# Optimization experiments

Measured on AMD Instinct MI355X. Metric: run time of the kernel, lower is better.

Reference implementation:

```python
import jax, jax.numpy as jnp
import numpy as np

B = 32          # number of trees (batch)
N_LEAVES = 512  # complete binary tree -> 2*N_LEAVES-1 nodes per tree
IN_DIM = 1024
MEM = 1024


def setup_inputs() -> dict:
    key = jax.random.key(0)
    k1, k2, k3, k4 = jax.random.split(key, 4)
    s = 0.02
    inputs = jax.random.normal(k1, (B, N_LEAVES, IN_DIM), jnp.float32)
    w_fioux = jax.random.normal(k2, (4 * MEM, IN_DIM), jnp.float32) * s
    # rand_init: bias zero except first mem_dim entries set to 1 (forget-gate bias)
    b_fioux = jnp.zeros((4 * MEM,), jnp.float32).at[:MEM].set(1.0)
    w_iouh = jax.random.normal(k3, (3 * MEM, 2 * MEM), jnp.float32) * s
    w_fh = jax.random.normal(k4, (2 * MEM, 2 * MEM), jnp.float32) * s
    return {"inputs": inputs, "w_fioux": w_fioux, "b_fioux": b_fioux,
            "w_iouh": w_iouh, "w_fh": w_fh}


def _node_forward(x, child_c, child_h, w_fioux, b_fioux, w_iouh, w_fh):
    # x: [B, n, IN_DIM]; child_c/child_h: [B, n, 2*MEM] (left || right)
    fioux = x @ w_fioux.T + b_fioux                      # [B, n, 4M]
    fx, ix, ox, ux = jnp.split(fioux, 4, axis=-1)        # each [B, n, M]
    ih, oh, uh = jnp.split(child_h @ w_iouh.T, 3, axis=-1)
    i = jax.nn.sigmoid(ix + ih)
    o = jax.nn.sigmoid(ox + oh)
    u = jnp.tanh(ux + uh)
    # f gates: fx repeated for both children + fh(child_h)
    f = jax.nn.sigmoid(jnp.concatenate([fx, fx], axis=-1) + child_h @ w_fh.T)
    fc = f * child_c                                     # [B, n, 2M]
    c = i * u + fc[..., :MEM] + fc[..., MEM:]            # sum over the 2 children
    h = o * jnp.tanh(c)
    return c, h


def reference(inputs, w_fioux, b_fioux, w_iouh, w_fh):
    # Leaves: x = word input, child states are zeros
    z = jnp.zeros((B, N_LEAVES, 2 * MEM), inputs.dtype)
    c, h = _node_forward(inputs, z, z, w_fioux, b_fioux, w_iouh, w_fh)
    n = N_LEAVES
    # Internal nodes, level by level (log2(N_LEAVES) fixed iterations):
    # x = zeros (internal nodes have no token input), children are adjacent pairs.
    while n > 1:
        n //= 2
        child_c = c.reshape(B, n, 2 * MEM)   # [left_c || right_c]
        child_h = h.reshape(B, n, 2 * MEM)
        x = jnp.zeros((B, n, IN_DIM), inputs.dtype)
        c, h = _node_forward(x, child_c, child_h, w_fioux, b_fioux, w_iouh, w_fh)
    return h[:, 0, :]  # root hidden state, [B, MEM]
```

## Files before the change

kernel.cpp:

```cpp
#include <hip/hip_runtime.h>
#include <cstdint>
#include <cstddef>


typedef __attribute__((ext_vector_type(8))) short bf16x8;
typedef __attribute__((ext_vector_type(4))) float f32x4;

__device__ __forceinline__ float sig_(float x) { return 1.0f / (1.0f + __expf(-x)); }

__device__ __forceinline__ unsigned short f2bf_(float x) {
    union { float f; uint32_t u; } v; v.f = x;
    uint32_t r = v.u + 0x7fffu + ((v.u >> 16) & 1u);
    return (unsigned short)(r >> 16);
}
__device__ __forceinline__ float bf2f_(unsigned short u) {
    union { uint32_t u; float f; } v; v.u = ((uint32_t)u) << 16; return v.f;
}

#define GL16(g, l) __builtin_amdgcn_global_load_lds( \
    (const __attribute__((address_space(1))) void*)(g), \
    (__attribute__((address_space(3))) void*)(l), 16, 0, 0)

__global__ __launch_bounds__(512, 2)
void gemm384f(const unsigned short* __restrict__ A,
              const unsigned short* __restrict__ Wp,
              const float* __restrict__ b,
              unsigned short* __restrict__ c_out,
              unsigned short* __restrict__ h_out,
              int M)
{
    __shared__ unsigned short lA[4 * 4096];
    __shared__ unsigned short lB[4 * 12288];
    const int lda = 1024;

    const int orig = blockIdx.x + 8 * blockIdx.y;
    const int bx = orig & 7;
    const int by = orig >> 3;

    const int tid = threadIdx.x;
    const int ln  = tid & 63;
    const int wv  = tid >> 6;
    const int wrp = wv >> 2;
    const int wcp = wv & 3;
    const int row0 = by * 128;
    const int colb = bx * 384;

    const int rowS = tid >> 2;
    const int gS   = (tid & 3) ^ ((tid >> 3) & 3);
    const unsigned short* a0 = A + (size_t)min(row0 + rowS, M - 1) * lda + gS * 8;
    const unsigned short* w0 = Wp + (size_t)(colb + rowS)       * lda + gS * 8;
    const unsigned short* w1 = Wp + (size_t)(colb + rowS + 128) * lda + gS * 8;
    const unsigned short* w2 = Wp + (size_t)(colb + rowS + 256) * lda + gS * 8;
    const int ld0 = tid * 8;
    const int ld1 = tid * 8 + 4096;
    const int ld2 = tid * 8 + 8192;

    int offA[4], offB[6];
    #pragma unroll
    for (int i = 0; i < 4; ++i) {
        const int r = wrp * 64 + i * 16 + (ln & 15);
        offA[i] = r * 32 + ((ln >> 4) ^ ((r >> 1) & 3)) * 8;
    }
    #pragma unroll
    for (int h = 0; h < 2; ++h)
        #pragma unroll
        for (int g = 0; g < 3; ++g) {
            const int r = h * 192 + g * 64 + wcp * 16 + (ln & 15);
            offB[h * 3 + g] = r * 32 + ((ln >> 4) ^ ((r >> 1) & 3)) * 8;
        }

    f32x4 acc[4][6] = {};
    const int P = 32;

#define ISSUE_L(kh) do { \
    const int _sl = (kh) & 3; \
    const size_t _ko = (size_t)(kh) * 32; \
    GL16(a0 + _ko, lA + _sl * 4096 + ld0); \
    GL16(w0 + _ko, lB + _sl * 12288 + ld0); \
    GL16(w1 + _ko, lB + _sl * 12288 + ld1); \
    GL16(w2 + _ko, lB + _sl * 12288 + ld2); \
} while (0)

    ISSUE_L(0); ISSUE_L(1); ISSUE_L(2);
    asm volatile("s_waitcnt vmcnt(8)" ::: "memory");
    asm volatile("s_barrier" ::: "memory");

    for (int p = 0; p < P; ++p) {
        const unsigned short* pa = lA + (p & 3) * 4096;
        const unsigned short* pb = lB + (p & 3) * 12288;
        bf16x8 bf[6], af[4];
        #pragma unroll
        for (int i = 0; i < 6; ++i) bf[i] = *(const bf16x8*)(pb + offB[i]);
        #pragma unroll
        for (int i = 0; i < 4; ++i) af[i] = *(const bf16x8*)(pa + offA[i]);
        if (p <= P - 4) ISSUE_L(p + 3);
        __builtin_amdgcn_s_setprio(1);
        #pragma unroll
        for (int m = 0; m < 4; ++m)
            #pragma unroll
            for (int g = 0; g < 6; ++g)
                acc[m][g] = __builtin_amdgcn_mfma_f32_16x16x32_bf16(af[m], bf[g], acc[m][g], 0, 0, 0);
        __builtin_amdgcn_s_setprio(0);
        if (p <= P - 4)      asm volatile("s_waitcnt vmcnt(8)" ::: "memory");
        else if (p == P - 3) asm volatile("s_waitcnt vmcnt(4)" ::: "memory");
        else if (p == P - 2) asm volatile("s_waitcnt vmcnt(0)" ::: "memory");
        if (p < P - 1) asm volatile("s_barrier" ::: "memory");
    }
#undef ISSUE_L

    #pragma unroll
    for (int h = 0; h < 2; ++h) {
        const int j = bx * 128 + h * 64 + wcp * 16 + (ln & 15);
        const float bi = b[1024 + j];
        const float bo = b[2048 + j];
        const float bu = b[3072 + j];
        #pragma unroll
        for (int mi = 0; mi < 4; ++mi) {
            #pragma unroll
            for (int rg = 0; rg < 4; ++rg) {
                const int r = row0 + wrp * 64 + mi * 16 + (ln >> 4) * 4 + rg;
                if (r < M) {
                    const float cv = sig_(acc[mi][h * 3 + 0][rg] + bi) * tanhf(acc[mi][h * 3 + 2][rg] + bu);
                    const float hv = sig_(acc[mi][h * 3 + 1][rg] + bo) * tanhf(cv);
                    c_out[(size_t)r * 1024 + j] = f2bf_(cv);
                    h_out[(size_t)r * 1024 + j] = f2bf_(hv);
                }
            }
        }
    }
}

__global__ __launch_bounds__(512, 2)
void gemm320f(const unsigned short* __restrict__ A,
              const unsigned short* __restrict__ Wp,
              const float* __restrict__ b,
              const unsigned short* __restrict__ c_prev,
              unsigned short* __restrict__ c_out,
              unsigned short* __restrict__ h_out,
              int M)
{
    __shared__ unsigned short lA[4 * 8192];
    __shared__ unsigned short lB[4 * 10240];
    const int lda = 2048;

    const int orig = blockIdx.x + 16 * blockIdx.y;
    const int xcd  = orig & 7;
    const int pos  = orig >> 3;
    const int bx   = xcd * 2 + (pos & 1);
    const int by   = pos >> 1;

    const int tid = threadIdx.x;
    const int ln  = tid & 63;
    const int wv  = tid >> 6;
    const int wrp = wv >> 2;
    const int wcp = wv & 3;
    const int row0 = by * 256;
    const int colb = bx * 320;
    const bool five = (wv < 4);

    const int rowS = tid >> 2;
    const int gS   = (tid & 3) ^ ((tid >> 3) & 3);
    const unsigned short* a0 = A + (size_t)min(row0 + rowS,       M - 1) * lda + gS * 8;
    const unsigned short* a1 = A + (size_t)min(row0 + rowS + 128, M - 1) * lda + gS * 8;
    const unsigned short* w0 = Wp + (size_t)(colb + rowS)       * lda + gS * 8;
    const unsigned short* w1 = Wp + (size_t)(colb + rowS + 128) * lda + gS * 8;
    const unsigned short* w2 = Wp + (size_t)(colb + 256 + ((tid & 255) >> 2)) * lda + gS * 8;
    const int ld0 = tid * 8;
    const int ld1 = tid * 8 + 4096;
    const int ld2 = (tid & 255) * 8 + 8192;

    int offA[8], offB[5];
    #pragma unroll
    for (int i = 0; i < 8; ++i) {
        const int r = wrp * 128 + i * 16 + (ln & 15);
        offA[i] = r * 32 + ((ln >> 4) ^ ((r >> 1) & 3)) * 8;
    }
    #pragma unroll
    for (int g = 0; g < 5; ++g) {
        const int r = g * 64 + wcp * 16 + (ln & 15);
        offB[g] = r * 32 + ((ln >> 4) ^ ((r >> 1) & 3)) * 8;
    }

    f32x4 acc[8][5] = {};
    const int P = 64;

#define ISSUE_F(kh) do { \
    const int _sl = (kh) & 3; \
    const size_t _ko = (size_t)(kh) * 32; \
    GL16(a0 + _ko, lA + _sl * 8192 + ld0); \
    GL16(a1 + _ko, lA + _sl * 8192 + ld1); \
    GL16(w0 + _ko, lB + _sl * 10240 + ld0); \
    GL16(w1 + _ko, lB + _sl * 10240 + ld1); \
    if (five) GL16(w2 + _ko, lB + _sl * 10240 + ld2); \
} while (0)

    ISSUE_F(0); ISSUE_F(1); ISSUE_F(2);
    if (five) asm volatile("s_waitcnt vmcnt(10)" ::: "memory");
    else      asm volatile("s_waitcnt vmcnt(8)"  ::: "memory");
    asm volatile("s_barrier" ::: "memory");

    for (int p = 0; p < P; ++p) {
        const unsigned short* pa = lA + (p & 3) * 8192;
        const unsigned short* pb = lB + (p & 3) * 10240;
        bf16x8 bf[5], af[4], ag[4];
        #pragma unroll
        for (int g = 0; g < 5; ++g) bf[g] = *(const bf16x8*)(pb + offB[g]);
        #pragma unroll
        for (int i = 0; i < 4; ++i) af[i] = *(const bf16x8*)(pa + offA[i]);
        #pragma unroll
        for (int i = 0; i < 4; ++i) ag[i] = *(const bf16x8*)(pa + offA[4 + i]);
        if (p <= P - 4) ISSUE_F(p + 3);
        __builtin_amdgcn_s_setprio(1);
        #pragma unroll
        for (int m = 0; m < 4; ++m)
            #pragma unroll
            for (int g = 0; g < 5; ++g)
                acc[m][g] = __builtin_amdgcn_mfma_f32_16x16x32_bf16(af[m], bf[g], acc[m][g], 0, 0, 0);
        #pragma unroll
        for (int m = 0; m < 4; ++m)
            #pragma unroll
            for (int g = 0; g < 5; ++g)
                acc[4 + m][g] = __builtin_amdgcn_mfma_f32_16x16x32_bf16(ag[m], bf[g], acc[4 + m][g], 0, 0, 0);
        __builtin_amdgcn_s_setprio(0);
        if (p <= P - 4) {
            if (five) asm volatile("s_waitcnt vmcnt(10)" ::: "memory");
            else      asm volatile("s_waitcnt vmcnt(8)"  ::: "memory");
        } else if (p == P - 3) {
            if (five) asm volatile("s_waitcnt vmcnt(5)" ::: "memory");
            else      asm volatile("s_waitcnt vmcnt(4)" ::: "memory");
        } else if (p == P - 2) {
            asm volatile("s_waitcnt vmcnt(0)" ::: "memory");
        }
        if (p < P - 1) asm volatile("s_barrier" ::: "memory");
    }
#undef ISSUE_F

    const int jg = bx * 64 + wcp * 16 + (ln & 15);
    const float bi = b[1024 + jg];
    const float bo = b[2048 + jg];
    const float bu = b[3072 + jg];
    const float bff = b[jg];
    #pragma unroll
    for (int mi = 0; mi < 8; ++mi) {
        #pragma unroll
        for (int rg = 0; rg < 4; ++rg) {
            const int r = row0 + wrp * 128 + mi * 16 + (ln >> 4) * 4 + rg;
            if (r < M) {
                const float cl = bf2f_(c_prev[(size_t)r * 2048 + jg]);
                const float cr = bf2f_(c_prev[(size_t)r * 2048 + 1024 + jg]);
                const float iv = sig_(acc[mi][0][rg] + bi);
                const float ov = sig_(acc[mi][1][rg] + bo);
                const float uv = tanhf(acc[mi][2][rg] + bu);
                const float flv = sig_(acc[mi][3][rg] + bff);
                const float frv = sig_(acc[mi][4][rg] + bff);
                const float c = iv * uv + flv * cl + frv * cr;
                const float h = ov * tanhf(c);
                c_out[(size_t)r * 1024 + jg] = f2bf_(c);
                h_out[(size_t)r * 1024 + jg] = f2bf_(h);
            }
        }
    }
}

__global__ __launch_bounds__(512, 2)
void gemm256(const unsigned short* __restrict__ A,
             const unsigned short* __restrict__ W,
             unsigned short* __restrict__ C, int M, int N, int lda, int Klen)
{
    __shared__ unsigned short lA[4 * 8192];
    __shared__ unsigned short lB[4 * 8192];

    const int gx = gridDim.x, gy = gridDim.y;
    int id = blockIdx.x + gx * (blockIdx.y + gy * blockIdx.z);
    {
        const int nwg = gx * gy * gridDim.z;
        const int q = nwg >> 3, r = nwg & 7, x = id & 7, i = id >> 3;
        id = (x < r ? x * (q + 1) : r * (q + 1) + (x - r) * q) + i;
    }
    const int bz  = id / (gx * gy);
    const int rem = id - bz * gx * gy;
    const int by  = rem / gx;
    const int bx  = rem - by * gx;

    const int tid = threadIdx.x;
    const int ln  = tid & 63;
    const int wv  = tid >> 6;
    const int wrp = wv >> 2;
    const int wcp = wv & 3;
    const int row0 = by * 256;
    const int colb = bx * 256;
    const int kbase = bz * Klen;
    C += (size_t)bz * M * N;

    const int rowS = tid >> 2;
    const int gS   = (tid & 3) ^ ((tid >> 3) & 3);
    const unsigned short* a0 = A + (size_t)min(row0 + rowS,       M - 1) * lda + kbase + gS * 8;
    const unsigned short* a1 = A + (size_t)min(row0 + rowS + 128, M - 1) * lda + kbase + gS * 8;
    const unsigned short* b0 = W + (size_t)(colb + rowS)       * lda + kbase + gS * 8;
    const unsigned short* b1 = W + (size_t)(colb + rowS + 128) * lda + kbase + gS * 8;
    const int ld0 = tid * 8;
    const int ld1 = tid * 8 + 4096;

    int offA[8], offB[4];
    #pragma unroll
    for (int i = 0; i < 8; ++i) {
        const int r = wrp * 128 + i * 16 + (ln & 15);
        offA[i] = r * 32 + ((ln >> 4) ^ ((r >> 1) & 3)) * 8;
    }
    #pragma unroll
    for (int i = 0; i < 4; ++i) {
        const int r = wcp * 64 + i * 16 + (ln & 15);
        offB[i] = r * 32 + ((ln >> 4) ^ ((r >> 1) & 3)) * 8;
    }

    f32x4 acc[8][4] = {};
    const int P = Klen >> 5;

#define ISSUE_KH(kh) do { \
    const int _sl = (kh) & 3; \
    const size_t _ko = (size_t)(kh) * 32; \
    GL16(a0 + _ko, lA + _sl * 8192 + ld0); \
    GL16(a1 + _ko, lA + _sl * 8192 + ld1); \
    GL16(b0 + _ko, lB + _sl * 8192 + ld0); \
    GL16(b1 + _ko, lB + _sl * 8192 + ld1); \
} while (0)

    ISSUE_KH(0); ISSUE_KH(1); ISSUE_KH(2);
    asm volatile("s_waitcnt vmcnt(8)" ::: "memory");
    asm volatile("s_barrier" ::: "memory");

    for (int p = 0; p < P; ++p) {
        const unsigned short* pa = lA + (p & 3) * 8192;
        const unsigned short* pb = lB + (p & 3) * 8192;
        bf16x8 bf[4], af[4], ag[4];
        #pragma unroll
        for (int i = 0; i < 4; ++i) bf[i] = *(const bf16x8*)(pb + offB[i]);
        #pragma unroll
        for (int i = 0; i < 4; ++i) af[i] = *(const bf16x8*)(pa + offA[i]);
        #pragma unroll
        for (int i = 0; i < 4; ++i) ag[i] = *(const bf16x8*)(pa + offA[4 + i]);
        if (p <= P - 4) ISSUE_KH(p + 3);
        __builtin_amdgcn_s_setprio(1);
        #pragma unroll
        for (int m = 0; m < 4; ++m)
            #pragma unroll
            for (int n = 0; n < 4; ++n)
                acc[m][n] = __builtin_amdgcn_mfma_f32_16x16x32_bf16(af[m], bf[n], acc[m][n], 0, 0, 0);
        #pragma unroll
        for (int m = 0; m < 4; ++m)
            #pragma unroll
            for (int n = 0; n < 4; ++n)
                acc[4 + m][n] = __builtin_amdgcn_mfma_f32_16x16x32_bf16(ag[m], bf[n], acc[4 + m][n], 0, 0, 0);
        __builtin_amdgcn_s_setprio(0);
        if (p <= P - 4)      asm volatile("s_waitcnt vmcnt(8)" ::: "memory");
        else if (p == P - 3) asm volatile("s_waitcnt vmcnt(4)" ::: "memory");
        else if (p == P - 2) asm volatile("s_waitcnt vmcnt(0)" ::: "memory");
        if (p < P - 1) asm volatile("s_barrier" ::: "memory");
    }
#undef ISSUE_KH

    #pragma unroll
    for (int mi = 0; mi < 8; ++mi) {
        #pragma unroll
        for (int ni = 0; ni < 4; ++ni) {
            const int col = colb + wcp * 64 + ni * 16 + (ln & 15);
            #pragma unroll
            for (int rg = 0; rg < 4; ++rg) {
                const int r = row0 + wrp * 128 + mi * 16 + (ln >> 4) * 4 + rg;
                if (r < M) C[(size_t)r * N + col] = f2bf_(acc[mi][ni][rg]);
            }
        }
    }
}

__global__ void f2bf_vec(const float* __restrict__ src, unsigned short* __restrict__ dst, int n4)
{
    const int i = blockIdx.x * blockDim.x + threadIdx.x;
    if (i >= n4) return;
    const float4 v = ((const float4*)src)[i];
    ushort4 o;
    o.x = f2bf_(v.x); o.y = f2bf_(v.y); o.z = f2bf_(v.z); o.w = f2bf_(v.w);
    ((ushort4*)dst)[i] = o;
}

__global__ void build_wfxp(const float* __restrict__ w_fioux,
                           unsigned short* __restrict__ dst, int total4)
{
    const int idx = blockIdx.x * blockDim.x + threadIdx.x;
    if (idx >= total4) return;
    const int rp = idx >> 8;
    const int c4 = (idx & 255) << 2;
    const int t  = rp / 192;
    const int q  = rp - t * 192;
    const int g  = q >> 6;
    const int jj = q & 63;
    const float* src = w_fioux + (size_t)((g + 1) * 1024 + t * 64 + jj) * 1024;
    const float4 v = *(const float4*)(src + c4);
    ushort4 o;
    o.x = f2bf_(v.x); o.y = f2bf_(v.y); o.z = f2bf_(v.z); o.w = f2bf_(v.w);
    *(ushort4*)(dst + (size_t)rp * 1024 + c4) = o;
}

__global__ void build_wcatp(const float* __restrict__ w_iouh, const float* __restrict__ w_fh,
                            unsigned short* __restrict__ dst, int total4)
{
    const int idx = blockIdx.x * blockDim.x + threadIdx.x;
    if (idx >= total4) return;
    const int rp = idx >> 9;
    const int c4 = (idx & 511) << 2;
    const int t  = rp / 320;
    const int q  = rp - t * 320;
    const int g  = q >> 6;
    const int jj = q & 63;
    const int srow = t * 64 + jj;
    const float* src = (g < 3) ? (w_iouh + (size_t)(g * 1024 + srow) * 2048)
                               : (w_fh   + (size_t)((g - 3) * 1024 + srow) * 2048);
    const float4 v = *(const float4*)(src + c4);
    ushort4 o;
    o.x = f2bf_(v.x); o.y = f2bf_(v.y); o.z = f2bf_(v.z); o.w = f2bf_(v.w);
    *(ushort4*)(dst + (size_t)rp * 2048 + c4) = o;
}

__device__ __forceinline__ void acc4_(float* v, ushort4 u) {
    v[0] += bf2f_(u.x); v[1] += bf2f_(u.y); v[2] += bf2f_(u.z); v[3] += bf2f_(u.w);
}

__global__ void node_gates(const unsigned short* __restrict__ g, int S, size_t sstride,
                           const float* __restrict__ b,
                           const unsigned short* __restrict__ c_prev,
                           unsigned short* __restrict__ c_out,
                           unsigned short* __restrict__ h_bf,
                           float* __restrict__ h_f32, int rows)
{
    const int idx = blockIdx.x * blockDim.x + threadIdx.x;
    if (idx >= rows * 256) return;
    const int r = idx >> 8, q = (idx & 255) << 2;
    const int t = q >> 6, jj = q & 63;
    float vi[4] = {}, vo[4] = {}, vu[4] = {}, vfl[4] = {}, vfr[4] = {};
    const unsigned short* gr = g + (size_t)r * 5120 + t * 320 + jj;
    for (int s = 0; s < S; ++s, gr += sstride) {
        acc4_(vi,  *(const ushort4*)(gr));
        acc4_(vo,  *(const ushort4*)(gr + 64));
        acc4_(vu,  *(const ushort4*)(gr + 128));
        acc4_(vfl, *(const ushort4*)(gr + 192));
        acc4_(vfr, *(const ushort4*)(gr + 256));
    }
    const float* bi = b + 1024 + q;
    const float* bo = b + 2048 + q;
    const float* bu = b + 3072 + q;
    const float* bff = b + q;
    const ushort4 clu = *(const ushort4*)(c_prev + (size_t)r * 2048 + q);
    const ushort4 cru = *(const ushort4*)(c_prev + (size_t)r * 2048 + 1024 + q);
    const float cl[4] = { bf2f_(clu.x), bf2f_(clu.y), bf2f_(clu.z), bf2f_(clu.w) };
    const float cr[4] = { bf2f_(cru.x), bf2f_(cru.y), bf2f_(cru.z), bf2f_(cru.w) };

    ushort4 co, ho;
    float cv[4], hv[4];
    #pragma unroll
    for (int e = 0; e < 4; ++e) {
        const float c = sig_(vi[e] + bi[e]) * tanhf(vu[e] + bu[e])
                      + sig_(vfl[e] + bff[e]) * cl[e]
                      + sig_(vfr[e] + bff[e]) * cr[e];
        cv[e] = c;
        hv[e] = sig_(vo[e] + bo[e]) * tanhf(c);
    }
    co.x = f2bf_(cv[0]); co.y = f2bf_(cv[1]); co.z = f2bf_(cv[2]); co.w = f2bf_(cv[3]);
    ho.x = f2bf_(hv[0]); ho.y = f2bf_(hv[1]); ho.z = f2bf_(hv[2]); ho.w = f2bf_(hv[3]);
    *(ushort4*)(c_out + (size_t)r * 1024 + q) = co;
    *(ushort4*)(h_bf + (size_t)r * 1024 + q) = ho;
    if (h_f32) {
        float4 hf; hf.x = hv[0]; hf.y = hv[1]; hf.z = hv[2]; hf.w = hv[3];
        *(float4*)(h_f32 + (size_t)r * 1024 + q) = hf;
    }
}

extern "C" void kernel_launch(void* const* d_in, const int* in_sizes, int n_in,
                              void* d_out, int out_size, void* d_ws, size_t ws_size,
                              hipStream_t stream)
{
    const float* inputs  = (const float*)d_in[0];
    const float* w_fioux = (const float*)d_in[1];
    const float* b_fioux = (const float*)d_in[2];
    const float* w_iouh  = (const float*)d_in[3];
    const float* w_fh    = (const float*)d_in[4];
    float* out = (float*)d_out;

    unsigned short* us    = (unsigned short*)d_ws;
    unsigned short* c_a   = us;
    unsigned short* c_b   = c_a + (size_t)16777216;
    unsigned short* h_a   = c_b + (size_t)8388608;
    unsigned short* h_b   = h_a + (size_t)16777216;
    unsigned short* wfxP  = h_b + (size_t)8388608;
    unsigned short* wcatP = wfxP + (size_t)3145728;
    unsigned short* gbuf  = wcatP + (size_t)10485760;
    unsigned short* x_bf  = gbuf;

    f2bf_vec<<<16384, 256, 0, stream>>>(inputs, x_bf, 4194304);
    build_wfxp<<<3072, 256, 0, stream>>>(w_fioux, wfxP, 786432);
    build_wcatp<<<10240, 256, 0, stream>>>(w_iouh, w_fh, wcatP, 5120 * 512);

    gemm384f<<<dim3(8, 128), 512, 0, stream>>>(x_bf, wfxP, b_fioux, c_a, h_a, 16384);

    unsigned short *hp = h_a, *cp = c_a, *hn = h_b, *cn = c_b;
    for (int n = 256; n >= 64; n >>= 1) {
        const int m = 32 * n;
        gemm320f<<<dim3(16, m / 256), 512, 0, stream>>>(hp, wcatP, b_fioux, cp, cn, hn, m);
        unsigned short* t;
        t = hp; hp = hn; hn = t;
        t = cp; cp = cn; cn = t;
    }

    for (int n = 32; n >= 1; n >>= 1) {
        const int m = 32 * n;
        const int S = (m >= 512) ? 4 : 8;
        const int Klen = 2048 / S;
        gemm256<<<dim3(20, (m + 255) / 256, S), 512, 0, stream>>>(
            hp, wcatP, gbuf, m, 5120, 2048, Klen);
        node_gates<<<m, 256, 0, stream>>>(
            gbuf, S, (size_t)m * 5120, b_fioux, cp, cn, hn,
            (n == 1) ? out : nullptr, m);
        unsigned short* t;
        t = hp; hp = hn; hn = t;
        t = cp; cp = cn; cn = t;
    }
    (void)in_sizes; (void)n_in; (void)out_size; (void)ws_size;
}
```

Before: 693.6 us.

## Shrink fused GEMM tiles to 256-thread blocks with 3-stage pipeline and finer gate interleave

Replaces the leaf and internal-node fused GEMM+gate kernels with smaller-tile versions: 256 threads, 128-row tiles, 192 or 160 columns, and a 3-slot LDS ring with prefetch distance 2 instead of 4 slots and distance 3. The packed weight layouts are re-interleaved in 16-column gate groups to match, and node_gates is updated for the new layout. It also adds XCD-aware block remapping and an s_sleep stagger for half the blocks. The aim is more blocks in flight and smaller LDS per block for better occupancy and load balance, at the cost of less data reuse per tile and a shallower prefetch.

```diff
diff --git a/kernel.cpp b/kernel.cpp
--- a/kernel.cpp
+++ b/kernel.cpp
@@ -21,242 +21,234 @@
     (const __attribute__((address_space(1))) void*)(g), \
     (__attribute__((address_space(3))) void*)(l), 16, 0, 0)
 
-__global__ __launch_bounds__(512, 2)
-void gemm384f(const unsigned short* __restrict__ A,
-              const unsigned short* __restrict__ Wp,
-              const float* __restrict__ b,
-              unsigned short* __restrict__ c_out,
-              unsigned short* __restrict__ h_out,
-              int M)
-{
-    __shared__ unsigned short lA[4 * 4096];
-    __shared__ unsigned short lB[4 * 12288];
-    const int lda = 1024;
-
-    const int orig = blockIdx.x + 8 * blockIdx.y;
-    const int bx = orig & 7;
-    const int by = orig >> 3;
+__global__ __launch_bounds__(256, 2)
+void gemm_nodef(const unsigned short* __restrict__ A,
+                const unsigned short* __restrict__ Wp,
+                const float* __restrict__ b,
+                const unsigned short* __restrict__ c_prev,
+                unsigned short* __restrict__ c_out,
+                unsigned short* __restrict__ h_out,
+                int M)
+{
+    __shared__ unsigned short lA[3 * 4096];
+    __shared__ unsigned short lB[3 * 5120];
+    const int lda = 2048;
+
+    const int orig = blockIdx.x + 32 * blockIdx.y;
+    const int xcd  = orig & 7;
+    const int pos  = orig >> 3;
+    const int bx   = xcd * 4 + (pos & 3);
+    const int by   = pos >> 2;
+
+    if ((pos >> 5) & 1) asm volatile("s_sleep 10" ::: "memory");
 
     const int tid = threadIdx.x;
     const int ln  = tid & 63;
     const int wv  = tid >> 6;
-    const int wrp = wv >> 2;
-    const int wcp = wv & 3;
+    const int wrp = wv >> 1;
+    const int wcp = wv & 1;
     const int row0 = by * 128;
-    const int colb = bx * 384;
+    const int colb = bx * 160;
+    const bool five = (wv < 2);
 
     const int rowS = tid >> 2;
     const int gS   = (tid & 3) ^ ((tid >> 3) & 3);
-    const unsigned short* a0 = A + (size_t)min(row0 + rowS, M - 1) * lda + gS * 8;
-    const unsigned short* w0 = Wp + (size_t)(colb + rowS)       * lda + gS * 8;
-    const unsigned short* w1 = Wp + (size_t)(colb + rowS + 128) * lda + gS * 8;
-    const unsigned short* w2 = Wp + (size_t)(colb + rowS + 256) * lda + gS * 8;
+    const unsigned short* a0 = A + (size_t)(row0 + rowS) * lda + gS * 8;
+    const unsigned short* a1 = a0 + (size_t)64 * lda;
+    const unsigned short* w0 = Wp + (size_t)(colb + rowS) * lda + gS * 8;
+    const unsigned short* w1 = w0 + (size_t)64 * lda;
+    const unsigned short* w2 = w0 + (size_t)128 * lda;
     const int ld0 = tid * 8;
-    const int ld1 = tid * 8 + 4096;
-    const int ld2 = tid * 8 + 8192;
-
-    int offA[4], offB[6];
+
+    int offA[4], offB[5];
     #pragma unroll
     for (int i = 0; i < 4; ++i) {
         const int r = wrp * 64 + i * 16 + (ln & 15);
         offA[i] = r * 32 + ((ln >> 4) ^ ((r >> 1) & 3)) * 8;
     }
     #pragma unroll
-    for (int h = 0; h < 2; ++h)
-        #pragma unroll
-        for (int g = 0; g < 3; ++g) {
-            const int r = h * 192 + g * 64 + wcp * 16 + (ln & 15);
-            offB[h * 3 + g] = r * 32 + ((ln >> 4) ^ ((r >> 1) & 3)) * 8;
-        }
-
-    f32x4 acc[4][6] = {};
-    const int P = 32;
-
-#define ISSUE_L(kh) do { \
-    const int _sl = (kh) & 3; \
+    for (int g = 0; g < 5; ++g) {
+        const int r = wcp * 80 + g * 16 + (ln & 15);
+        offB[g] = r * 32 + ((ln >> 4) ^ ((r >> 1) & 3)) * 8;
+    }
+
+    f32x4 acc[4][5] = {};
+    const int P = 64;
+
+#define ISSUE_N(sl, kh) do { \
     const size_t _ko = (size_t)(kh) * 32; \
-    GL16(a0 + _ko, lA + _sl * 4096 + ld0); \
-    GL16(w0 + _ko, lB + _sl * 12288 + ld0); \
-    GL16(w1 + _ko, lB + _sl * 12288 + ld1); \
-    GL16(w2 + _ko, lB + _sl * 12288 + ld2); \
+    GL16(a0 + _ko, lA + (sl) * 4096 + ld0); \
+    GL16(a1 + _ko, lA + (sl) * 4096 + 2048 + ld0); \
+    GL16(w0 + _ko, lB + (sl) * 5120 + ld0); \
+    GL16(w1 + _ko, lB + (sl) * 5120 + 2048 + ld0); \
+    if (five) GL16(w2 + _ko, lB + (sl) * 5120 + 4096 + ld0); \
 } while (0)
 
-    ISSUE_L(0); ISSUE_L(1); ISSUE_L(2);
-    asm volatile("s_waitcnt vmcnt(8)" ::: "memory");
+    ISSUE_N(0, 0); ISSUE_N(1, 1);
+    if (five) asm volatile("s_waitcnt vmcnt(5)" ::: "memory");
+    else      asm volatile("s_waitcnt vmcnt(4)" ::: "memory");
     asm volatile("s_barrier" ::: "memory");
 
+    int rd = 0, is = 2;
     for (int p = 0; p < P; ++p) {
-        const unsigned short* pa = lA + (p & 3) * 4096;
-        const unsigned short* pb = lB + (p & 3) * 12288;
-        bf16x8 bf[6], af[4];
-        #pragma unroll
-        for (int i = 0; i < 6; ++i) bf[i] = *(const bf16x8*)(pb + offB[i]);
+        const unsigned short* pa = lA + rd * 4096;
+        const unsigned short* pb = lB + rd * 5120;
+        bf16x8 bf[5], af[4];
+        #pragma unroll
+        for (int g = 0; g < 5; ++g) bf[g] = *(const bf16x8*)(pb + offB[g]);
         #pragma unroll
         for (int i = 0; i < 4; ++i) af[i] = *(const bf16x8*)(pa + offA[i]);
-        if (p <= P - 4) ISSUE_L(p + 3);
-        __builtin_amdgcn_s_setprio(1);
-        #pragma unroll
-        for (int m = 0; m < 4; ++m)
-            #pragma unroll
-            for (int g = 0; g < 6; ++g)
-                acc[m][g] = __builtin_amdgcn_mfma_f32_16x16x32_bf16(af[m], bf[g], acc[m][g], 0, 0, 0);
-        __builtin_amdgcn_s_setprio(0);
-        if (p <= P - 4)      asm volatile("s_waitcnt vmcnt(8)" ::: "memory");
-        else if (p == P - 3) asm volatile("s_waitcnt vmcnt(4)" ::: "memory");
-        else if (p == P - 2) asm volatile("s_waitcnt vmcnt(0)" ::: "memory");
-        if (p < P - 1) asm volatile("s_barrier" ::: "memory");
-    }
-#undef ISSUE_L
-
-    #pragma unroll
-    for (int h = 0; h < 2; ++h) {
-        const int j = bx * 128 + h * 64 + wcp * 16 + (ln & 15);
-        const float bi = b[1024 + j];
-        const float bo = b[2048 + j];
-        const float bu = b[3072 + j];
-        #pragma unroll
-        for (int mi = 0; mi < 4; ++mi) {
-            #pragma unroll
-            for (int rg = 0; rg < 4; ++rg) {
-                const int r = row0 + wrp * 64 + mi * 16 + (ln >> 4) * 4 + rg;
-                if (r < M) {
-                    const float cv = sig_(acc[mi][h * 3 + 0][rg] + bi) * tanhf(acc[mi][h * 3 + 2][rg] + bu);
-                    const float hv = sig_(acc[mi][h * 3 + 1][rg] + bo) * tanhf(cv);
-                    c_out[(size_t)r * 1024 + j] = f2bf_(cv);
-                    h_out[(size_t)r * 1024 + j] = f2bf_(hv);
-                }
-            }
-        }
-    }
-}
-
-__global__ __launch_bounds__(512, 2)
-void gemm320f(const unsigned short* __restrict__ A,
-              const unsigned short* __restrict__ Wp,
-              const float* __restrict__ b,
-              const unsigned short* __restrict__ c_prev,
-              unsigned short* __restrict__ c_out,
-              unsigned short* __restrict__ h_out,
-              int M)
-{
-    __shared__ unsigned short lA[4 * 8192];
-    __shared__ unsigned short lB[4 * 10240];
-    const int lda = 2048;
-
-    const int orig = blockIdx.x + 16 * blockIdx.y;
-    const int xcd  = orig & 7;
-    const int pos  = orig >> 3;
-    const int bx   = xcd * 2 + (pos & 1);
-    const int by   = pos >> 1;
-
-    const int tid = threadIdx.x;
-    const int ln  = tid & 63;
-    const int wv  = tid >> 6;
-    const int wrp = wv >> 2;
-    const int wcp = wv & 3;
-    const int row0 = by * 256;
-    const int colb = bx * 320;
-    const bool five = (wv < 4);
-
-    const int rowS = tid >> 2;
-    const int gS   = (tid & 3) ^ ((tid >> 3) & 3);
-    const unsigned short* a0 = A + (size_t)min(row0 + rowS,       M - 1) * lda + gS * 8;
-    const unsigned short* a1 = A + (size_t)min(row0 + rowS + 128, M - 1) * lda + gS * 8;
-    const unsigned short* w0 = Wp + (size_t)(colb + rowS)       * lda + gS * 8;
-    const unsigned short* w1 = Wp + (size_t)(colb + rowS + 128) * lda + gS * 8;
-    const unsigned short* w2 = Wp + (size_t)(colb + 256 + ((tid & 255) >> 2)) * lda + gS * 8;
-    const int ld0 = tid * 8;
-    const int ld1 = tid * 8 + 4096;
-    const int ld2 = (tid & 255) * 8 + 8192;
-
-    int offA[8], offB[5];
-    #pragma unroll
-    for (int i = 0; i < 8; ++i) {
-        const int r = wrp * 128 + i * 16 + (ln & 15);
-        offA[i] = r * 32 + ((ln >> 4) ^ ((r >> 1) & 3)) * 8;
-    }
-    #pragma unroll
-    for (int g = 0; g < 5; ++g) {
-        const int r = g * 64 + wcp * 16 + (ln & 15);
-        offB[g] = r * 32 + ((ln >> 4) ^ ((r >> 1) & 3)) * 8;
-    }
-
-    f32x4 acc[8][5] = {};
-    const int P = 64;
-
-#define ISSUE_F(kh) do { \
-    const int _sl = (kh) & 3; \
-    const size_t _ko = (size_t)(kh) * 32; \
-    GL16(a0 + _ko, lA + _sl * 8192 + ld0); \
-    GL16(a1 + _ko, lA + _sl * 8192 + ld1); \
-    GL16(w0 + _ko, lB + _sl * 10240 + ld0); \
-    GL16(w1 + _ko, lB + _sl * 10240 + ld1); \
-    if (five) GL16(w2 + _ko, lB + _sl * 10240 + ld2); \
-} while (0)
-
-    ISSUE_F(0); ISSUE_F(1); ISSUE_F(2);
-    if (five) asm volatile("s_waitcnt vmcnt(10)" ::: "memory");
-    else      asm volatile("s_waitcnt vmcnt(8)"  ::: "memory");
-    asm volatile("s_barrier" ::: "memory");
-
-    for (int p = 0; p < P; ++p) {
-        const unsigned short* pa = lA + (p & 3) * 8192;
-        const unsigned short* pb = lB + (p & 3) * 10240;
-        bf16x8 bf[5], af[4], ag[4];
-        #pragma unroll
-        for (int g = 0; g < 5; ++g) bf[g] = *(const bf16x8*)(pb + offB[g]);
-        #pragma unroll
-        for (int i = 0; i < 4; ++i) af[i] = *(const bf16x8*)(pa + offA[i]);
-        #pragma unroll
-        for (int i = 0; i < 4; ++i) ag[i] = *(const bf16x8*)(pa + offA[4 + i]);
-        if (p <= P - 4) ISSUE_F(p + 3);
+        if (p <= P - 3) ISSUE_N(is, p + 2);
         __builtin_amdgcn_s_setprio(1);
         #pragma unroll
         for (int m = 0; m < 4; ++m)
             #pragma unroll
             for (int g = 0; g < 5; ++g)
                 acc[m][g] = __builtin_amdgcn_mfma_f32_16x16x32_bf16(af[m], bf[g], acc[m][g], 0, 0, 0);
-        #pragma unroll
-        for (int m = 0; m < 4; ++m)
-            #pragma unroll
-            for (int g = 0; g < 5; ++g)
-                acc[4 + m][g] = __builtin_amdgcn_mfma_f32_16x16x32_bf16(ag[m], bf[g], acc[4 + m][g], 0, 0, 0);
         __builtin_amdgcn_s_setprio(0);
-        if (p <= P - 4) {
-            if (five) asm volatile("s_waitcnt vmcnt(10)" ::: "memory");
-            else      asm volatile("s_waitcnt vmcnt(8)"  ::: "memory");
-        } else if (p == P - 3) {
+        if (p <= P - 3) {
             if (five) asm volatile("s_waitcnt vmcnt(5)" ::: "memory");
             else      asm volatile("s_waitcnt vmcnt(4)" ::: "memory");
         } else if (p == P - 2) {
             asm volatile("s_waitcnt vmcnt(0)" ::: "memory");
         }
         if (p < P - 1) asm volatile("s_barrier" ::: "memory");
-    }
-#undef ISSUE_F
-
-    const int jg = bx * 64 + wcp * 16 + (ln & 15);
+        rd = (rd == 2) ? 0 : rd + 1;
+        is = (is == 2) ? 0 : is + 1;
+    }
+#undef ISSUE_N
+
+    const int jg = bx * 32 + wcp * 16 + (ln & 15);
     const float bi = b[1024 + jg];
     const float bo = b[2048 + jg];
     const float bu = b[3072 + jg];
     const float bff = b[jg];
     #pragma unroll
-    for (int mi = 0; mi < 8; ++mi) {
+    for (int mi = 0; mi < 4; ++mi) {
         #pragma unroll
         for (int rg = 0; rg < 4; ++rg) {
-            const int r = row0 + wrp * 128 + mi * 16 + (ln >> 4) * 4 + rg;
-            if (r < M) {
-                const float cl = bf2f_(c_prev[(size_t)r * 2048 + jg]);
-                const float cr = bf2f_(c_prev[(size_t)r * 2048 + 1024 + jg]);
-                const float iv = sig_(acc[mi][0][rg] + bi);
-                const float ov = sig_(acc[mi][1][rg] + bo);
-                const float uv = tanhf(acc[mi][2][rg] + bu);
-                const float flv = sig_(acc[mi][3][rg] + bff);
-                const float frv = sig_(acc[mi][4][rg] + bff);
-                const float c = iv * uv + flv * cl + frv * cr;
-                const float h = ov * tanhf(c);
-                c_out[(size_t)r * 1024 + jg] = f2bf_(c);
-                h_out[(size_t)r * 1024 + jg] = f2bf_(h);
+            const int r = row0 + wrp * 64 + mi * 16 + (ln >> 4) * 4 + rg;
+            const float cl = bf2f_(c_prev[(size_t)r * 2048 + jg]);
+            const float cr = bf2f_(c_prev[(size_t)r * 2048 + 1024 + jg]);
+            const float iv = sig_(acc[mi][0][rg] + bi);
+            const float ov = sig_(acc[mi][1][rg] + bo);
+            const float uv = tanhf(acc[mi][2][rg] + bu);
+            const float flv = sig_(acc[mi][3][rg] + bff);
+            const float frv = sig_(acc[mi][4][rg] + bff);
+            const float c = iv * uv + flv * cl + frv * cr;
+            const float h = ov * tanhf(c);
+            c_out[(size_t)r * 1024 + jg] = f2bf_(c);
+            h_out[(size_t)r * 1024 + jg] = f2bf_(h);
+        }
+    }
+}
+
+__global__ __launch_bounds__(256, 2)
+void gemm_leaff(const unsigned short* __restrict__ A,
+                const unsigned short* __restrict__ Wp,
+                const float* __restrict__ b,
+                unsigned short* __restrict__ c_out,
+                unsigned short* __restrict__ h_out)
+{
+    __shared__ unsigned short lA[3 * 4096];
+    __shared__ unsigned short lB[3 * 6144];
+    const int lda = 1024;
+
+    const int orig = blockIdx.x + 16 * blockIdx.y;
+    const int xcd  = orig & 7;
+    const int pos  = orig >> 3;
+    const int bx   = xcd * 2 + (pos & 1);
+    const int by   = pos >> 1;
+
+    if ((pos >> 5) & 1) asm volatile("s_sleep 10" ::: "memory");
+
+    const int tid = threadIdx.x;
+    const int ln  = tid & 63;
+    const int wv  = tid >> 6;
+    const int wrp = wv >> 1;
+    const int wcp = wv & 1;
+    const int row0 = by * 128;
+    const int colb = bx * 192;
+
+    const int rowS = tid >> 2;
+    const int gS   = (tid & 3) ^ ((tid >> 3) & 3);
+    const unsigned short* a0 = A + (size_t)(row0 + rowS) * lda + gS * 8;
+    const unsigned short* a1 = a0 + (size_t)64 * lda;
+    const unsigned short* w0 = Wp + (size_t)(colb + rowS) * lda + gS * 8;
+    const unsigned short* w1 = w0 + (size_t)64 * lda;
+    const unsigned short* w2 = w0 + (size_t)128 * lda;
+    const int ld0 = tid * 8;
+
+    int offA[4], offB[6];
+    #pragma unroll
+    for (int i = 0; i < 4; ++i) {
+        const int r = wrp * 64 + i * 16 + (ln & 15);
+        offA[i] = r * 32 + ((ln >> 4) ^ ((r >> 1) & 3)) * 8;
+    }
+    #pragma unroll
+    for (int grp = 0; grp < 2; ++grp)
+        #pragma unroll
+        for (int g = 0; g < 3; ++g) {
+            const int r = wcp * 96 + grp * 48 + g * 16 + (ln & 15);
+            offB[grp * 3 + g] = r * 32 + ((ln >> 4) ^ ((r >> 1) & 3)) * 8;
+        }
+
+    f32x4 acc[4][6] = {};
+    const int P = 32;
+
+#define ISSUE_L(sl, kh) do { \
+    const size_t _ko = (size_t)(kh) * 32; \
+    GL16(a0 + _ko, lA + (sl) * 4096 + ld0); \
+    GL16(a1 + _ko, lA + (sl) * 4096 + 2048 + ld0); \
+    GL16(w0 + _ko, lB + (sl) * 6144 + ld0); \
+    GL16(w1 + _ko, lB + (sl) * 6144 + 2048 + ld0); \
+    GL16(w2 + _ko, lB + (sl) * 6144 + 4096 + ld0); \
+} while (0)
+
+    ISSUE_L(0, 0); ISSUE_L(1, 1);
+    asm volatile("s_waitcnt vmcnt(5)" ::: "memory");
+    asm volatile("s_barrier" ::: "memory");
+
+    int rd = 0, is = 2;
+    for (int p = 0; p < P; ++p) {
+        const unsigned short* pa = lA + rd * 4096;
+        const unsigned short* pb = lB + rd * 6144;
+        bf16x8 bf[6], af[4];
+        #pragma unroll
+        for (int g = 0; g < 6; ++g) bf[g] = *(const bf16x8*)(pb + offB[g]);
+        #pragma unroll
+        for (int i = 0; i < 4; ++i) af[i] = *(const bf16x8*)(pa + offA[i]);
+        if (p <= P - 3) ISSUE_L(is, p + 2);
+        __builtin_amdgcn_s_setprio(1);
+        #pragma unroll
+        for (int m = 0; m < 4; ++m)
+            #pragma unroll
+            for (int g = 0; g < 6; ++g)
+                acc[m][g] = __builtin_amdgcn_mfma_f32_16x16x32_bf16(af[m], bf[g], acc[m][g], 0, 0, 0);
+        __builtin_amdgcn_s_setprio(0);
+        if (p <= P - 3)      asm volatile("s_waitcnt vmcnt(5)" ::: "memory");
+        else if (p == P - 2) asm volatile("s_waitcnt vmcnt(0)" ::: "memory");
+        if (p < P - 1) asm volatile("s_barrier" ::: "memory");
+        rd = (rd == 2) ? 0 : rd + 1;
+        is = (is == 2) ? 0 : is + 1;
+    }
+#undef ISSUE_L
+
+    #pragma unroll
+    for (int grp = 0; grp < 2; ++grp) {
+        const int j = bx * 64 + wcp * 32 + grp * 16 + (ln & 15);
+        const float bi = b[1024 + j];
+        const float bo = b[2048 + j];
+        const float bu = b[3072 + j];
+        #pragma unroll
+        for (int mi = 0; mi < 4; ++mi) {
+            #pragma unroll
+            for (int rg = 0; rg < 4; ++rg) {
+                const int r = row0 + wrp * 64 + mi * 16 + (ln >> 4) * 4 + rg;
+                const float cv = sig_(acc[mi][grp * 3 + 0][rg] + bi) * tanhf(acc[mi][grp * 3 + 2][rg] + bu);
+                const float hv = sig_(acc[mi][grp * 3 + 1][rg] + bo) * tanhf(cv);
+                c_out[(size_t)r * 1024 + j] = f2bf_(cv);
+                h_out[(size_t)r * 1024 + j] = f2bf_(hv);
             }
         }
     }
@@ -390,11 +382,11 @@
     if (idx >= total4) return;
     const int rp = idx >> 8;
     const int c4 = (idx & 255) << 2;
-    const int t  = rp / 192;
-    const int q  = rp - t * 192;
-    const int g  = q >> 6;
-    const int jj = q & 63;
-    const float* src = w_fioux + (size_t)((g + 1) * 1024 + t * 64 + jj) * 1024;
+    const int t  = rp / 48;
+    const int q  = rp - t * 48;
+    const int g  = q >> 4;
+    const int jj = q & 15;
+    const float* src = w_fioux + (size_t)((g + 1) * 1024 + t * 16 + jj) * 1024;
     const float4 v = *(const float4*)(src + c4);
     ushort4 o;
     o.x = f2bf_(v.x); o.y = f2bf_(v.y); o.z = f2bf_(v.z); o.w = f2bf_(v.w);
@@ -408,11 +400,11 @@
     if (idx >= total4) return;
     const int rp = idx >> 9;
     const int c4 = (idx & 511) << 2;
-    const int t  = rp / 320;
-    const int q  = rp - t * 320;
-    const int g  = q >> 6;
-    const int jj = q & 63;
-    const int srow = t * 64 + jj;
+    const int t  = rp / 80;
+    const int q  = rp - t * 80;
+    const int g  = q >> 4;
+    const int jj = q & 15;
+    const int srow = t * 16 + jj;
     const float* src = (g < 3) ? (w_iouh + (size_t)(g * 1024 + srow) * 2048)
                                : (w_fh   + (size_t)((g - 3) * 1024 + srow) * 2048);
     const float4 v = *(const float4*)(src + c4);
@@ -435,15 +427,15 @@
     const int idx = blockIdx.x * blockDim.x + threadIdx.x;
     if (idx >= rows * 256) return;
     const int r = idx >> 8, q = (idx & 255) << 2;
-    const int t = q >> 6, jj = q & 63;
+    const int t = q >> 4, jj = q & 15;
     float vi[4] = {}, vo[4] = {}, vu[4] = {}, vfl[4] = {}, vfr[4] = {};
-    const unsigned short* gr = g + (size_t)r * 5120 + t * 320 + jj;
+    const unsigned short* gr = g + (size_t)r * 5120 + t * 80 + jj;
     for (int s = 0; s < S; ++s, gr += sstride) {
         acc4_(vi,  *(const ushort4*)(gr));
-        acc4_(vo,  *(const ushort4*)(gr + 64));
-        acc4_(vu,  *(const ushort4*)(gr + 128));
-        acc4_(vfl, *(const ushort4*)(gr + 192));
-        acc4_(vfr, *(const ushort4*)(gr + 256));
+        acc4_(vo,  *(const ushort4*)(gr + 16));
+        acc4_(vu,  *(const ushort4*)(gr + 32));
+        acc4_(vfl, *(const ushort4*)(gr + 48));
+        acc4_(vfr, *(const ushort4*)(gr + 64));
     }
     const float* bi = b + 1024 + q;
     const float* bo = b + 2048 + q;
@@ -499,12 +491,12 @@
     build_wfxp<<<3072, 256, 0, stream>>>(w_fioux, wfxP, 786432);
     build_wcatp<<<10240, 256, 0, stream>>>(w_iouh, w_fh, wcatP, 5120 * 512);
 
-    gemm384f<<<dim3(8, 128), 512, 0, stream>>>(x_bf, wfxP, b_fioux, c_a, h_a, 16384);
+    gemm_leaff<<<dim3(16, 128), 256, 0, stream>>>(x_bf, wfxP, b_fioux, c_a, h_a);
 
     unsigned short *hp = h_a, *cp = c_a, *hn = h_b, *cn = c_b;
     for (int n = 256; n >= 64; n >>= 1) {
         const int m = 32 * n;
-        gemm320f<<<dim3(16, m / 256), 512, 0, stream>>>(hp, wcatP, b_fioux, cp, cn, hn, m);
+        gemm_nodef<<<dim3(32, m / 128), 256, 0, stream>>>(hp, wcatP, b_fioux, cp, cn, hn, m);
         unsigned short* t;
         t = hp; hp = hn; hn = t;
         t = cp; cp = cn; cn = t;
```

Result: no change. 687.8 us (-0.8%).
